# Performance work log

Measured on AMD Instinct MI355X. Metric: run time of the kernel, lower is better.

## Reference

```python
import jax, jax.numpy as jnp
import numpy as np

N_NODES = 65536
N_EDGES = 1048576


def gcn_conv(x, W, b, src, dst, n_nodes):
    """PyG GCNConv (normalize=True, add_self_loops already applied in src/dst):
    out = D^{-1/2} (A+I) D^{-1/2} X W + b, aggregated at dst (target) nodes."""
    deg = jax.ops.segment_sum(jnp.ones_like(dst, dtype=x.dtype), dst, num_segments=n_nodes)
    dis = jax.lax.rsqrt(jnp.maximum(deg, 1.0))  # self loops guarantee deg >= 1
    norm = dis[src] * dis[dst]                  # [E]
    h = x @ W                                   # [N, out]
    agg = jax.ops.segment_sum(h[src] * norm[:, None], dst, num_segments=n_nodes)
    return agg + b


def setup_inputs() -> dict:
    key = jax.random.key(0)
    ks = jax.random.split(key, 8)
    x = jax.random.normal(ks[0], (N_NODES, 128), dtype=jnp.float32)
    edge_index = jax.random.randint(ks[1], (2, N_EDGES), 0, N_NODES, dtype=jnp.int64)
    dims = [(128, 256), (256, 128), (128, 64)]
    params = {}
    for i, (din, dout) in enumerate(dims):
        scale = 1.0 / np.sqrt(din)
        params[f"W{i+1}"] = jax.random.uniform(ks[2 + i], (din, dout), dtype=jnp.float32, minval=-scale, maxval=scale)
        params[f"b{i+1}"] = jnp.zeros((dout,), dtype=jnp.float32)
    return {"x": x, "edge_index": edge_index, **params}


def reference(x, edge_index, W1, b1, W2, b2, W3, b3):
    n = x.shape[0]
    loop = jnp.arange(n, dtype=edge_index.dtype)
    src = jnp.concatenate([edge_index[0], loop])  # add self loops
    dst = jnp.concatenate([edge_index[1], loop])
    for W, b in ((W1, b1), (W2, b2), (W3, b3)):
        x = gcn_conv(x, W, b, src, dst, n)
        x = jax.nn.softmax(jax.nn.relu(x), axis=1)  # ReLU then Softmax(dim=1) per layer
    return x
```

## Files before the change

kernel.cpp:

```cpp
#include <hip/hip_runtime.h>
#include <cstdint>
#include <cstddef>

#define N_NODES 65536
#define N_EDGES 1048576
#define E_TOT   (N_EDGES + N_NODES)
#define CAP     5120

using short8  = __attribute__((ext_vector_type(8))) short;
using floatx4 = __attribute__((ext_vector_type(4))) float;
using half8   = __attribute__((ext_vector_type(8))) _Float16;
using half4   = __attribute__((ext_vector_type(4))) _Float16;
typedef unsigned short ushort_t;

__device__ inline void split_bf16(float a, short& hi, short& lo) {
    unsigned u  = __float_as_uint(a);
    unsigned hr = (u + 0x7fffu + ((u >> 16) & 1u)) >> 16;
    float    hf = __uint_as_float(hr << 16);
    hi = (short)hr;
    float    lf = a - hf;
    lo = (short)(__float_as_uint(lf) >> 16);
}


__global__ __launch_bounds__(1024) void k_bucket(const int* __restrict__ src, const int* __restrict__ dst,
                                                 int* __restrict__ gcur, unsigned* __restrict__ pk) {
    __shared__ int cnt[256];
    __shared__ int cur[256];
    int tid = threadIdx.x;
    if (tid < 256) cnt[tid] = 0;
    __syncthreads();
    int base = blockIdx.x * 4096;
    #pragma unroll
    for (int j = 0; j < 4; ++j) {
        int d = __builtin_nontemporal_load(&dst[base + j * 1024 + tid]);
        atomicAdd(&cnt[d >> 8], 1);
    }
    __syncthreads();
    if (tid < 256) cur[tid] = CAP * tid + atomicAdd(&gcur[tid], cnt[tid]);
    __syncthreads();
    #pragma unroll
    for (int j = 0; j < 4; ++j) {
        int e = base + j * 1024 + tid;
        int d = __builtin_nontemporal_load(&dst[e]);
        int s = __builtin_nontemporal_load(&src[e]);
        int pos = atomicAdd(&cur[d >> 8], 1);
        pk[pos] = ((unsigned)s << 16) | (unsigned)d;
    }
}

__global__ __launch_bounds__(256) void k_boff(const int* __restrict__ gcur, int* __restrict__ boff,
                                              int* __restrict__ off) {
    __shared__ int sb[256];
    int tid = threadIdx.x;
    int v = gcur[tid] + 256;
    sb[tid] = v;
    __syncthreads();
    #pragma unroll
    for (int s = 1; s < 256; s <<= 1) {
        int t = (tid >= s) ? sb[tid - s] : 0;
        __syncthreads();
        sb[tid] += t;
        __syncthreads();
    }
    boff[tid] = sb[tid] - v;
    if (tid == 255) boff[256] = sb[255];
    if (tid == 0) off[N_NODES] = E_TOT;
}

__global__ __launch_bounds__(1024) void k_sortb(const unsigned* __restrict__ pk, const int* __restrict__ gcur,
                                                const int* __restrict__ boff, int* __restrict__ off,
                                                float* __restrict__ dis, ushort_t* __restrict__ ssort) {
    __shared__ int cnt[256];
    __shared__ int sb[256];
    __shared__ int cur[256];
    int b = blockIdx.x;
    int tid = threadIdx.x;
    int n = gcur[b];
    const unsigned* p = pk + (size_t)b * CAP;
    if (tid < 256) cnt[tid] = 0;
    __syncthreads();
    for (int i = tid; i < n; i += 1024) atomicAdd(&cnt[p[i] & 255u], 1);
    __syncthreads();
    if (tid < 256) sb[tid] = cnt[tid];
    __syncthreads();
    #pragma unroll
    for (int s = 1; s < 256; s <<= 1) {
        int t = (tid < 256 && tid >= s) ? sb[tid - s] : 0;
        __syncthreads();
        if (tid < 256) sb[tid] += t;
        __syncthreads();
    }
    if (tid < 256) {
        int deg = cnt[tid];
        int o = boff[b] + (sb[tid] - deg) + tid;
        int d = b * 256 + tid;
        off[d] = o;
        dis[d] = rsqrtf((float)(deg + 1));
        ssort[o + deg] = (ushort_t)d;
        cur[tid] = o;
    }
    __syncthreads();
    for (int i = tid; i < n; i += 1024) {
        unsigned v = p[i];
        int pos = atomicAdd(&cur[v & 255u], 1);
        ssort[pos] = (ushort_t)(v >> 16);
    }
}


#define G1 (16 * 4 * 64)
#define G2 (8 * 8 * 64)
#define G3 (4 * 4 * 64)
#define NBX 8192
#define NBW ((G1 + G2 + G3 + 255) / 256)

__device__ inline void convw_split(const float* W, int K, int N, short* Bh, short* Bl, int g) {
    int lane = g & 63;
    int kt = (g >> 6) % (K / 32);
    int nt = (g >> 6) / (K / 32);
    int n = nt * 16 + (lane & 15);
    int kbase = kt * 32 + (lane >> 4) * 8;
    #pragma unroll
    for (int j = 0; j < 8; ++j) {
        short h, l;
        split_bf16(W[(size_t)(kbase + j) * N + n], h, l);
        Bh[(size_t)g * 8 + j] = h;
        Bl[(size_t)g * 8 + j] = l;
    }
}

__device__ inline void convw_h(const float* W, int K, int N, _Float16* Bf, int g) {
    int lane = g & 63;
    int kt = (g >> 6) % (K / 32);
    int nt = (g >> 6) / (K / 32);
    int n = nt * 16 + (lane & 15);
    int kbase = kt * 32 + (lane >> 4) * 8;
    #pragma unroll
    for (int j = 0; j < 8; ++j)
        Bf[(size_t)g * 8 + j] = (_Float16)W[(size_t)(kbase + j) * N + n];
}

__global__ __launch_bounds__(256) void k_fused(
        const float* __restrict__ x, const float* __restrict__ dis, _Float16* __restrict__ xh,
        const float* __restrict__ W1, short* __restrict__ w1h, short* __restrict__ w1l,
        const float* __restrict__ W2, _Float16* __restrict__ w2f,
        const float* __restrict__ W3, _Float16* __restrict__ w3f) {
    int b = blockIdx.x;
    if (b < NBX) {
        int idx = (b * 256 + threadIdx.x) * 4;
        int row = idx >> 7;
        float d = dis[row];
        float4 v = *(const float4*)(x + idx);
        half4 o = {(_Float16)(d * v.x), (_Float16)(d * v.y), (_Float16)(d * v.z), (_Float16)(d * v.w)};
        *(half4*)(xh + idx) = o;
    } else {
        int g = (b - NBX) * 256 + threadIdx.x;
        if (g < G1)                 convw_split(W1, 128, 256, w1h, w1l, g);
        else if (g < G1 + G2)       convw_h(W2, 256, 128, w2f, g - G1);
        else if (g < G1 + G2 + G3)  convw_h(W3, 128, 64, w3f, g - G1 - G2);
    }
}


template <int K, int N>
__global__ __launch_bounds__(256) void k_mms(const _Float16* __restrict__ A,
                                             const short* __restrict__ Bh, const short* __restrict__ Bl,
                                             const float* __restrict__ bias, _Float16* __restrict__ Cout) {
    constexpr int NT = N / 16;
    constexpr int KT = K / 32;
    int tid = threadIdx.x;
    int wave = tid >> 6, lane = tid & 63;
    int quad = lane >> 4, col = lane & 15;
    size_t row0 = (size_t)blockIdx.x * 64;
    const _Float16* ap = A + (row0 + wave * 16 + col) * K + quad * 8;

    floatx4 acc[NT];
    #pragma unroll
    for (int t = 0; t < NT; ++t) acc[t] = (floatx4)0.0f;

    for (int kt = 0; kt < KT; ++kt) {
        half8 a8 = *(const half8*)(ap + kt * 32);
        short ah[8], al[8];
        #pragma unroll
        for (int j = 0; j < 8; ++j) split_bf16((float)a8[j], ah[j], al[j]);
        short8 afh = *(short8*)ah;
        short8 afl = *(short8*)al;
        #pragma unroll
        for (int nt = 0; nt < NT; ++nt) {
            size_t bi = ((size_t)(nt * KT + kt) * 64 + lane);
            short8 bfh = ((const short8*)Bh)[bi];
            short8 bfl = ((const short8*)Bl)[bi];
            acc[nt] = __builtin_amdgcn_mfma_f32_16x16x32_bf16(afh, bfh, acc[nt], 0, 0, 0);
            acc[nt] = __builtin_amdgcn_mfma_f32_16x16x32_bf16(afh, bfl, acc[nt], 0, 0, 0);
            acc[nt] = __builtin_amdgcn_mfma_f32_16x16x32_bf16(afl, bfh, acc[nt], 0, 0, 0);
        }
    }

    size_t rbase = row0 + wave * 16 + quad * 4;
    float bv[NT];
    #pragma unroll
    for (int nt = 0; nt < NT; ++nt) bv[nt] = bias[nt * 16 + col];
    float mr[4] = {0.f, 0.f, 0.f, 0.f};
    #pragma unroll
    for (int nt = 0; nt < NT; ++nt)
        #pragma unroll
        for (int r = 0; r < 4; ++r) {
            float v = fmaxf(acc[nt][r] + bv[nt], 0.0f);
            acc[nt][r] = v;
            mr[r] = fmaxf(mr[r], v);
        }
    #pragma unroll
    for (int mask = 1; mask < 16; mask <<= 1)
        #pragma unroll
        for (int r = 0; r < 4; ++r) mr[r] = fmaxf(mr[r], __shfl_xor(mr[r], mask, 64));
    float sr[4] = {0.f, 0.f, 0.f, 0.f};
    #pragma unroll
    for (int nt = 0; nt < NT; ++nt)
        #pragma unroll
        for (int r = 0; r < 4; ++r) {
            float t = __expf(acc[nt][r] - mr[r]);
            acc[nt][r] = t;
            sr[r] += t;
        }
    #pragma unroll
    for (int mask = 1; mask < 16; mask <<= 1)
        #pragma unroll
        for (int r = 0; r < 4; ++r) sr[r] += __shfl_xor(sr[r], mask, 64);
    float inv[4];
    #pragma unroll
    for (int r = 0; r < 4; ++r) inv[r] = 1.0f / sr[r];
    #pragma unroll
    for (int nt = 0; nt < NT; ++nt)
        #pragma unroll
        for (int r = 0; r < 4; ++r)
            Cout[(rbase + r) * N + nt * 16 + col] = (_Float16)(acc[nt][r] * inv[r]);
}


template <int K, int N>
__global__ __launch_bounds__(256) void k_mmh(const _Float16* __restrict__ A,
                                             const _Float16* __restrict__ Bf,
                                             const float* __restrict__ dis, _Float16* __restrict__ Cout) {
    constexpr int NT = N / 16;
    constexpr int KT = K / 32;
    int tid = threadIdx.x;
    int wave = tid >> 6, lane = tid & 63;
    int quad = lane >> 4, col = lane & 15;
    size_t row0 = (size_t)blockIdx.x * 64;
    const _Float16* ap = A + (row0 + wave * 16 + col) * K + quad * 8;

    floatx4 acc[NT];
    #pragma unroll
    for (int t = 0; t < NT; ++t) acc[t] = (floatx4)0.0f;

    for (int kt = 0; kt < KT; ++kt) {
        half8 a8 = *(const half8*)(ap + kt * 32);
        #pragma unroll
        for (int nt = 0; nt < NT; ++nt) {
            half8 bf = ((const half8*)Bf)[(size_t)(nt * KT + kt) * 64 + lane];
            acc[nt] = __builtin_amdgcn_mfma_f32_16x16x32_f16(a8, bf, acc[nt], 0, 0, 0);
        }
    }

    size_t rbase = row0 + wave * 16 + quad * 4;
    float4 d4 = *(const float4*)(dis + rbase);
    float dr[4] = {d4.x, d4.y, d4.z, d4.w};
    #pragma unroll
    for (int nt = 0; nt < NT; ++nt)
        #pragma unroll
        for (int r = 0; r < 4; ++r)
            Cout[(rbase + r) * N + nt * 16 + col] = (_Float16)(acc[nt][r] * dr[r]);
}


template <bool ACT>
__global__ __launch_bounds__(256) void k_agg128h(const _Float16* __restrict__ h, const int* __restrict__ off,
                                                 const ushort_t* __restrict__ ss, const float* __restrict__ dis,
                                                 const float* __restrict__ bias, _Float16* __restrict__ out) {
    int lane = threadIdx.x & 63;
    int sub = lane >> 4;
    int li  = lane & 15;
    int c0  = li * 8;
    int n = blockIdx.x * 4 + (threadIdx.x >> 6);
    int e0 = off[n], e1 = off[n + 1];
    int e = e0;
    float acc[8];
    #pragma unroll
    for (int j = 0; j < 8; ++j) acc[j] = 0.0f;

    if (ACT) {
        half8 hacc = {0, 0, 0, 0, 0, 0, 0, 0};
        for (; e + 16 <= e1; e += 16) {
            int s0 = ss[e + sub];
            int s1 = ss[e + 4 + sub];
            int s2 = ss[e + 8 + sub];
            int s3 = ss[e + 12 + sub];
            half8 v0 = *(const half8*)(h + (size_t)s0 * 128 + c0);
            half8 v1 = *(const half8*)(h + (size_t)s1 * 128 + c0);
            half8 v2 = *(const half8*)(h + (size_t)s2 * 128 + c0);
            half8 v3 = *(const half8*)(h + (size_t)s3 * 128 + c0);
            hacc += (v0 + v1) + (v2 + v3);
        }
        for (; e + 8 <= e1; e += 8) {
            int sa = ss[e + sub];
            int sb = ss[e + 4 + sub];
            half8 va = *(const half8*)(h + (size_t)sa * 128 + c0);
            half8 vb = *(const half8*)(h + (size_t)sb * 128 + c0);
            hacc += va + vb;
        }
        #pragma unroll
        for (int j = 0; j < 8; ++j) acc[j] = (float)hacc[j];
    } else {
        for (; e + 16 <= e1; e += 16) {
            int s0 = ss[e + sub];
            int s1 = ss[e + 4 + sub];
            int s2 = ss[e + 8 + sub];
            int s3 = ss[e + 12 + sub];
            half8 v0 = *(const half8*)(h + (size_t)s0 * 128 + c0);
            half8 v1 = *(const half8*)(h + (size_t)s1 * 128 + c0);
            half8 v2 = *(const half8*)(h + (size_t)s2 * 128 + c0);
            half8 v3 = *(const half8*)(h + (size_t)s3 * 128 + c0);
            half8 vs = (v0 + v1) + (v2 + v3);
            #pragma unroll
            for (int j = 0; j < 8; ++j) acc[j] += (float)vs[j];
        }
        for (; e + 8 <= e1; e += 8) {
            int sa = ss[e + sub];
            int sb = ss[e + 4 + sub];
            half8 va = *(const half8*)(h + (size_t)sa * 128 + c0);
            half8 vb = *(const half8*)(h + (size_t)sb * 128 + c0);
            half8 vs = va + vb;
            #pragma unroll
            for (int j = 0; j < 8; ++j) acc[j] += (float)vs[j];
        }
    }
    while (e < e1) {
        int rem = e1 - e;
        int idx = e + sub;
        if (idx >= e1) idx = e1 - 1;
        int s = ss[idx];
        half8 v = *(const half8*)(h + (size_t)s * 128 + c0);
        float w = (sub < rem) ? 1.0f : 0.0f;
        #pragma unroll
        for (int j = 0; j < 8; ++j) acc[j] = fmaf(w, (float)v[j], acc[j]);
        e += 4;
    }

    #pragma unroll
    for (int mask = 32; mask >= 16; mask >>= 1)
        #pragma unroll
        for (int j = 0; j < 8; ++j) acc[j] += __shfl_xor(acc[j], mask, 64);

    float dn = dis[n];
    if (ACT) {
        float m = 0.0f;
        #pragma unroll
        for (int j = 0; j < 8; ++j) {
            float v = fmaxf(fmaf(acc[j], dn, bias[c0 + j]), 0.0f);
            acc[j] = v;
            m = fmaxf(m, v);
        }
        #pragma unroll
        for (int mask = 8; mask > 0; mask >>= 1) m = fmaxf(m, __shfl_xor(m, mask, 64));
        float sum = 0.0f;
        #pragma unroll
        for (int j = 0; j < 8; ++j) {
            float t = __expf(acc[j] - m);
            acc[j] = t;
            sum += t;
        }
        #pragma unroll
        for (int mask = 8; mask > 0; mask >>= 1) sum += __shfl_xor(sum, mask, 64);
        float inv = 1.0f / sum;
        #pragma unroll
        for (int j = 0; j < 8; ++j) acc[j] *= inv;
    } else {
        #pragma unroll
        for (int j = 0; j < 8; ++j) acc[j] *= dn;
    }
    if (sub == 0) {
        half8 o;
        #pragma unroll
        for (int j = 0; j < 8; ++j) o[j] = (_Float16)acc[j];
        *(half8*)(out + (size_t)n * 128 + c0) = o;
    }
}


__global__ __launch_bounds__(256) void k_agg64h(const _Float16* __restrict__ h, const int* __restrict__ off,
                                                const ushort_t* __restrict__ ss, const float* __restrict__ dis,
                                                const float* __restrict__ bias, float* __restrict__ out) {
    int lane = threadIdx.x & 63;
    int sub = lane >> 3;
    int li  = lane & 7;
    int c0  = li * 8;
    int n = blockIdx.x * 4 + (threadIdx.x >> 6);
    int e0 = off[n], e1 = off[n + 1];
    int e = e0;
    float acc[8];
    #pragma unroll
    for (int j = 0; j < 8; ++j) acc[j] = 0.0f;

    half8 hacc = {0, 0, 0, 0, 0, 0, 0, 0};
    for (; e + 16 <= e1; e += 16) {
        int s0 = ss[e + sub];
        int s1 = ss[e + 8 + sub];
        half8 v0 = *(const half8*)(h + (size_t)s0 * 64 + c0);
        half8 v1 = *(const half8*)(h + (size_t)s1 * 64 + c0);
        hacc += v0 + v1;
    }
    for (; e + 8 <= e1; e += 8) {
        int s = ss[e + sub];
        half8 v = *(const half8*)(h + (size_t)s * 64 + c0);
        hacc += v;
    }
    #pragma unroll
    for (int j = 0; j < 8; ++j) acc[j] = (float)hacc[j];

    int rem = e1 - e;
    if (rem > 0) {
        int idx = e + sub;
        if (idx >= e1) idx = e1 - 1;
        int s = ss[idx];
        half8 v = *(const half8*)(h + (size_t)s * 64 + c0);
        float w = (sub < rem) ? 1.0f : 0.0f;
        #pragma unroll
        for (int j = 0; j < 8; ++j) acc[j] = fmaf(w, (float)v[j], acc[j]);
    }

    #pragma unroll
    for (int mask = 32; mask >= 8; mask >>= 1)
        #pragma unroll
        for (int j = 0; j < 8; ++j) acc[j] += __shfl_xor(acc[j], mask, 64);

    float dn = dis[n];
    float m = 0.0f;
    #pragma unroll
    for (int j = 0; j < 8; ++j) {
        float v = fmaxf(fmaf(acc[j], dn, bias[c0 + j]), 0.0f);
        acc[j] = v;
        m = fmaxf(m, v);
    }
    #pragma unroll
    for (int mask = 4; mask > 0; mask >>= 1) m = fmaxf(m, __shfl_xor(m, mask, 64));
    float sum = 0.0f;
    #pragma unroll
    for (int j = 0; j < 8; ++j) {
        float t = __expf(acc[j] - m);
        acc[j] = t;
        sum += t;
    }
    #pragma unroll
    for (int mask = 4; mask > 0; mask >>= 1) sum += __shfl_xor(sum, mask, 64);
    float inv = 1.0f / sum;
    if (sub == 0) {
        float* op = out + (size_t)n * 64 + c0;
        *(float4*)(op)     = make_float4(acc[0] * inv, acc[1] * inv, acc[2] * inv, acc[3] * inv);
        *(float4*)(op + 4) = make_float4(acc[4] * inv, acc[5] * inv, acc[6] * inv, acc[7] * inv);
    }
}


extern "C" void kernel_launch(void* const* d_in, const int* in_sizes, int n_in,
                              void* d_out, int out_size, void* d_ws, size_t ws_size,
                              hipStream_t stream) {
    const float* x  = (const float*)d_in[0];
    const int*   ei = (const int*)d_in[1];
    const float* W1 = (const float*)d_in[2];
    const float* b1 = (const float*)d_in[3];
    const float* W2 = (const float*)d_in[4];
    const float* b2 = (const float*)d_in[5];
    const float* W3 = (const float*)d_in[6];
    const float* b3 = (const float*)d_in[7];
    const int* srcE = ei;
    const int* dstE = ei + N_EDGES;

    char* p = (char*)d_ws;
    auto carve = [&](size_t bytes) {
        char* q = p;
        p += (bytes + 255) & ~(size_t)255;
        return q;
    };
    int*          gcur  = (int*)carve(sizeof(int) * 256);
    int*          boff  = (int*)carve(sizeof(int) * 257);
    int*          off   = (int*)carve(sizeof(int) * (N_NODES + 1));
    float*        dis   = (float*)carve(sizeof(float) * N_NODES);
    unsigned*     pk    = (unsigned*)carve(sizeof(unsigned) * 256 * CAP);
    ushort_t*     ssort = (ushort_t*)carve(sizeof(ushort_t) * E_TOT);
    short*        w1h   = (short*)carve(sizeof(short) * 128 * 256);
    short*        w1l   = (short*)carve(sizeof(short) * 128 * 256);
    _Float16*     w2f   = (_Float16*)carve(sizeof(_Float16) * 256 * 128);
    _Float16*     w3f   = (_Float16*)carve(sizeof(_Float16) * 128 * 64);
    _Float16*     xh    = (_Float16*)carve(sizeof(_Float16) * (size_t)N_NODES * 128);
    _Float16*     a0h   = (_Float16*)carve(sizeof(_Float16) * (size_t)N_NODES * 128);
    _Float16*     x1h   = (_Float16*)carve(sizeof(_Float16) * (size_t)N_NODES * 256);
    _Float16*     x2h   = (_Float16*)carve(sizeof(_Float16) * (size_t)N_NODES * 128);
    _Float16*     hh    = (_Float16*)carve(sizeof(_Float16) * (size_t)N_NODES * 128);

    (void)hipMemsetAsync(gcur, 0, sizeof(int) * 256, stream);
    k_bucket<<<256, 1024, 0, stream>>>(srcE, dstE, gcur, pk);
    k_boff<<<1, 256, 0, stream>>>(gcur, boff, off);
    k_sortb<<<256, 1024, 0, stream>>>(pk, gcur, boff, off, dis, ssort);
    k_fused<<<NBX + NBW, 256, 0, stream>>>(x, dis, xh, W1, w1h, w1l, W2, w2f, W3, w3f);

    k_agg128h<false><<<N_NODES / 4, 256, 0, stream>>>(xh, off, ssort, dis, nullptr, a0h);
    k_mms<128, 256><<<N_NODES / 64, 256, 0, stream>>>(a0h, w1h, w1l, b1, x1h);
    k_mmh<256, 128><<<N_NODES / 64, 256, 0, stream>>>(x1h, w2f, dis, hh);
    k_agg128h<true><<<N_NODES / 4, 256, 0, stream>>>(hh, off, ssort, dis, b2, x2h);
    k_mmh<128, 64><<<N_NODES / 64, 256, 0, stream>>>(x2h, w3f, dis, hh);
    k_agg64h<<<N_NODES / 4, 256, 0, stream>>>(hh, off, ssort, dis, b3, (float*)d_out);
}
```

Baseline: 293.1 us.

## Slice feature matrices into 32-column planes for cache-friendly gather aggregation

Stores the 128-wide fp16 feature matrices as four 32-column slices (N x 32 each), so each aggregation block gathers only one slice. The working set per pass then fits in L2 and gathers become 64-byte rows. The activation (bias, ReLU, softmax) is moved out of the layer-2 aggregation into a separate k_act2 kernel. This adds an extra kernel launch and an extra intermediate buffer round-trip, and reads the CSR offsets and indices four times.

```diff
diff --git a/kernel.cpp b/kernel.cpp
--- a/kernel.cpp
+++ b/kernel.cpp
@@ -6,11 +6,13 @@
 #define N_EDGES 1048576
 #define E_TOT   (N_EDGES + N_NODES)
 #define CAP     5120
+#define SLICE_ELEMS ((size_t)N_NODES * 32)
 
 using short8  = __attribute__((ext_vector_type(8))) short;
 using floatx4 = __attribute__((ext_vector_type(4))) float;
 using half8   = __attribute__((ext_vector_type(8))) _Float16;
 using half4   = __attribute__((ext_vector_type(4))) _Float16;
+using half2v  = __attribute__((ext_vector_type(2))) _Float16;
 typedef unsigned short ushort_t;
 
 __device__ inline void split_bf16(float a, short& hi, short& lo) {
@@ -150,10 +152,11 @@
     if (b < NBX) {
         int idx = (b * 256 + threadIdx.x) * 4;
         int row = idx >> 7;
+        int c0 = idx & 127;
         float d = dis[row];
         float4 v = *(const float4*)(x + idx);
         half4 o = {(_Float16)(d * v.x), (_Float16)(d * v.y), (_Float16)(d * v.z), (_Float16)(d * v.w)};
-        *(half4*)(xh + idx) = o;
+        *(half4*)(xh + (size_t)(c0 >> 5) * SLICE_ELEMS + (size_t)row * 32 + (c0 & 31)) = o;
     } else {
         int g = (b - NBX) * 256 + threadIdx.x;
         if (g < G1)                 convw_split(W1, 128, 256, w1h, w1l, g);
@@ -238,7 +241,7 @@
 }
 
 
-template <int K, int N>
+template <int K, int N, bool SLICED>
 __global__ __launch_bounds__(256) void k_mmh(const _Float16* __restrict__ A,
                                              const _Float16* __restrict__ Bf,
                                              const float* __restrict__ dis, _Float16* __restrict__ Cout) {
@@ -269,122 +272,94 @@
     #pragma unroll
     for (int nt = 0; nt < NT; ++nt)
         #pragma unroll
-        for (int r = 0; r < 4; ++r)
-            Cout[(rbase + r) * N + nt * 16 + col] = (_Float16)(acc[nt][r] * dr[r]);
-}
-
-
-template <bool ACT>
-__global__ __launch_bounds__(256) void k_agg128h(const _Float16* __restrict__ h, const int* __restrict__ off,
-                                                 const ushort_t* __restrict__ ss, const float* __restrict__ dis,
-                                                 const float* __restrict__ bias, _Float16* __restrict__ out) {
+        for (int r = 0; r < 4; ++r) {
+            int c = nt * 16 + col;
+            _Float16 v = (_Float16)(acc[nt][r] * dr[r]);
+            if (SLICED)
+                Cout[(size_t)(c >> 5) * SLICE_ELEMS + (rbase + r) * 32 + (c & 31)] = v;
+            else
+                Cout[(rbase + r) * N + c] = v;
+        }
+}
+
+
+template <bool FP32ACC>
+__global__ __launch_bounds__(256) void k_aggs(const _Float16* __restrict__ h, const int* __restrict__ off,
+                                              const ushort_t* __restrict__ ss, const float* __restrict__ dis,
+                                              _Float16* __restrict__ out) {
+    int g = blockIdx.x & 7;
     int lane = threadIdx.x & 63;
-    int sub = lane >> 4;
-    int li  = lane & 15;
-    int c0  = li * 8;
+    int wave = threadIdx.x >> 6;
+    int sub = lane >> 3;
+    int li  = lane & 7;
+    const _Float16* hs = h + (size_t)g * SLICE_ELEMS + li * 4;
+    int nbase = (blockIdx.x >> 3) * 8 + wave * 2;
+
+    #pragma unroll
+    for (int k = 0; k < 2; ++k) {
+        int n = nbase + k;
+        int e0 = off[n], e1 = off[n + 1];
+        int e = e0;
+        float acc[4] = {0.f, 0.f, 0.f, 0.f};
+        if (FP32ACC) {
+            for (; e + 8 <= e1; e += 8) {
+                int s = ss[e + sub];
+                half4 v = *(const half4*)(hs + (size_t)s * 32);
+                #pragma unroll
+                for (int j = 0; j < 4; ++j) acc[j] += (float)v[j];
+            }
+        } else {
+            half4 hacc = {0, 0, 0, 0};
+            for (; e + 8 <= e1; e += 8) {
+                int s = ss[e + sub];
+                half4 v = *(const half4*)(hs + (size_t)s * 32);
+                hacc += v;
+            }
+            #pragma unroll
+            for (int j = 0; j < 4; ++j) acc[j] = (float)hacc[j];
+        }
+        int rem = e1 - e;
+        if (rem > 0) {
+            int idx = e + sub;
+            if (idx >= e1) idx = e1 - 1;
+            int s = ss[idx];
+            half4 v = *(const half4*)(hs + (size_t)s * 32);
+            float w = (sub < rem) ? 1.0f : 0.0f;
+            #pragma unroll
+            for (int j = 0; j < 4; ++j) acc[j] = fmaf(w, (float)v[j], acc[j]);
+        }
+        #pragma unroll
+        for (int mask = 32; mask >= 8; mask >>= 1)
+            #pragma unroll
+            for (int j = 0; j < 4; ++j) acc[j] += __shfl_xor(acc[j], mask, 64);
+        float dn = dis[n];
+        if (sub == 0) {
+            half4 o = {(_Float16)(acc[0] * dn), (_Float16)(acc[1] * dn),
+                       (_Float16)(acc[2] * dn), (_Float16)(acc[3] * dn)};
+            *(half4*)(out + (size_t)n * 128 + g * 32 + li * 4) = o;
+        }
+    }
+}
+
+
+__global__ __launch_bounds__(256) void k_act2(const _Float16* __restrict__ z, const float* __restrict__ bias,
+                                              _Float16* __restrict__ out) {
+    int lane = threadIdx.x & 63;
     int n = blockIdx.x * 4 + (threadIdx.x >> 6);
-    int e0 = off[n], e1 = off[n + 1];
-    int e = e0;
-    float acc[8];
-    #pragma unroll
-    for (int j = 0; j < 8; ++j) acc[j] = 0.0f;
-
-    if (ACT) {
-        half8 hacc = {0, 0, 0, 0, 0, 0, 0, 0};
-        for (; e + 16 <= e1; e += 16) {
-            int s0 = ss[e + sub];
-            int s1 = ss[e + 4 + sub];
-            int s2 = ss[e + 8 + sub];
-            int s3 = ss[e + 12 + sub];
-            half8 v0 = *(const half8*)(h + (size_t)s0 * 128 + c0);
-            half8 v1 = *(const half8*)(h + (size_t)s1 * 128 + c0);
-            half8 v2 = *(const half8*)(h + (size_t)s2 * 128 + c0);
-            half8 v3 = *(const half8*)(h + (size_t)s3 * 128 + c0);
-            hacc += (v0 + v1) + (v2 + v3);
-        }
-        for (; e + 8 <= e1; e += 8) {
-            int sa = ss[e + sub];
-            int sb = ss[e + 4 + sub];
-            half8 va = *(const half8*)(h + (size_t)sa * 128 + c0);
-            half8 vb = *(const half8*)(h + (size_t)sb * 128 + c0);
-            hacc += va + vb;
-        }
-        #pragma unroll
-        for (int j = 0; j < 8; ++j) acc[j] = (float)hacc[j];
-    } else {
-        for (; e + 16 <= e1; e += 16) {
-            int s0 = ss[e + sub];
-            int s1 = ss[e + 4 + sub];
-            int s2 = ss[e + 8 + sub];
-            int s3 = ss[e + 12 + sub];
-            half8 v0 = *(const half8*)(h + (size_t)s0 * 128 + c0);
-            half8 v1 = *(const half8*)(h + (size_t)s1 * 128 + c0);
-            half8 v2 = *(const half8*)(h + (size_t)s2 * 128 + c0);
-            half8 v3 = *(const half8*)(h + (size_t)s3 * 128 + c0);
-            half8 vs = (v0 + v1) + (v2 + v3);
-            #pragma unroll
-            for (int j = 0; j < 8; ++j) acc[j] += (float)vs[j];
-        }
-        for (; e + 8 <= e1; e += 8) {
-            int sa = ss[e + sub];
-            int sb = ss[e + 4 + sub];
-            half8 va = *(const half8*)(h + (size_t)sa * 128 + c0);
-            half8 vb = *(const half8*)(h + (size_t)sb * 128 + c0);
-            half8 vs = va + vb;
-            #pragma unroll
-            for (int j = 0; j < 8; ++j) acc[j] += (float)vs[j];
-        }
-    }
-    while (e < e1) {
-        int rem = e1 - e;
-        int idx = e + sub;
-        if (idx >= e1) idx = e1 - 1;
-        int s = ss[idx];
-        half8 v = *(const half8*)(h + (size_t)s * 128 + c0);
-        float w = (sub < rem) ? 1.0f : 0.0f;
-        #pragma unroll
-        for (int j = 0; j < 8; ++j) acc[j] = fmaf(w, (float)v[j], acc[j]);
-        e += 4;
-    }
-
-    #pragma unroll
-    for (int mask = 32; mask >= 16; mask >>= 1)
-        #pragma unroll
-        for (int j = 0; j < 8; ++j) acc[j] += __shfl_xor(acc[j], mask, 64);
-
-    float dn = dis[n];
-    if (ACT) {
-        float m = 0.0f;
-        #pragma unroll
-        for (int j = 0; j < 8; ++j) {
-            float v = fmaxf(fmaf(acc[j], dn, bias[c0 + j]), 0.0f);
-            acc[j] = v;
-            m = fmaxf(m, v);
-        }
-        #pragma unroll
-        for (int mask = 8; mask > 0; mask >>= 1) m = fmaxf(m, __shfl_xor(m, mask, 64));
-        float sum = 0.0f;
-        #pragma unroll
-        for (int j = 0; j < 8; ++j) {
-            float t = __expf(acc[j] - m);
-            acc[j] = t;
-            sum += t;
-        }
-        #pragma unroll
-        for (int mask = 8; mask > 0; mask >>= 1) sum += __shfl_xor(sum, mask, 64);
-        float inv = 1.0f / sum;
-        #pragma unroll
-        for (int j = 0; j < 8; ++j) acc[j] *= inv;
-    } else {
-        #pragma unroll
-        for (int j = 0; j < 8; ++j) acc[j] *= dn;
-    }
-    if (sub == 0) {
-        half8 o;
-        #pragma unroll
-        for (int j = 0; j < 8; ++j) o[j] = (_Float16)acc[j];
-        *(half8*)(out + (size_t)n * 128 + c0) = o;
-    }
+    int c0 = lane * 2;
+    half2v z2 = *(const half2v*)(z + (size_t)n * 128 + c0);
+    float v0 = fmaxf((float)z2[0] + bias[c0], 0.0f);
+    float v1 = fmaxf((float)z2[1] + bias[c0 + 1], 0.0f);
+    float m = fmaxf(v0, v1);
+    #pragma unroll
+    for (int mask = 32; mask > 0; mask >>= 1) m = fmaxf(m, __shfl_xor(m, mask, 64));
+    float t0 = __expf(v0 - m), t1 = __expf(v1 - m);
+    float sum = t0 + t1;
+    #pragma unroll
+    for (int mask = 32; mask > 0; mask >>= 1) sum += __shfl_xor(sum, mask, 64);
+    float inv = 1.0f / sum;
+    half2v o = {(_Float16)(t0 * inv), (_Float16)(t1 * inv)};
+    *(half2v*)(out + (size_t)n * 128 + c0) = o;
 }
 
 
@@ -496,6 +471,7 @@
     _Float16*     a0h   = (_Float16*)carve(sizeof(_Float16) * (size_t)N_NODES * 128);
     _Float16*     x1h   = (_Float16*)carve(sizeof(_Float16) * (size_t)N_NODES * 256);
     _Float16*     x2h   = (_Float16*)carve(sizeof(_Float16) * (size_t)N_NODES * 128);
+    _Float16*     zz    = (_Float16*)carve(sizeof(_Float16) * (size_t)N_NODES * 128);
     _Float16*     hh    = (_Float16*)carve(sizeof(_Float16) * (size_t)N_NODES * 128);
 
     (void)hipMemsetAsync(gcur, 0, sizeof(int) * 256, stream);
@@ -504,10 +480,11 @@
     k_sortb<<<256, 1024, 0, stream>>>(pk, gcur, boff, off, dis, ssort);
     k_fused<<<NBX + NBW, 256, 0, stream>>>(x, dis, xh, W1, w1h, w1l, W2, w2f, W3, w3f);
 
-    k_agg128h<false><<<N_NODES / 4, 256, 0, stream>>>(xh, off, ssort, dis, nullptr, a0h);
+    k_aggs<true><<<8 * (N_NODES / 8), 256, 0, stream>>>(xh, off, ssort, dis, a0h);
     k_mms<128, 256><<<N_NODES / 64, 256, 0, stream>>>(a0h, w1h, w1l, b1, x1h);
-    k_mmh<256, 128><<<N_NODES / 64, 256, 0, stream>>>(x1h, w2f, dis, hh);
-    k_agg128h<true><<<N_NODES / 4, 256, 0, stream>>>(hh, off, ssort, dis, b2, x2h);
-    k_mmh<128, 64><<<N_NODES / 64, 256, 0, stream>>>(x2h, w3f, dis, hh);
+    k_mmh<256, 128, true><<<N_NODES / 64, 256, 0, stream>>>(x1h, w2f, dis, hh);
+    k_aggs<false><<<8 * (N_NODES / 8), 256, 0, stream>>>(hh, off, ssort, dis, zz);
+    k_act2<<<N_NODES / 4, 256, 0, stream>>>(zz, b2, x2h);
+    k_mmh<128, 64, false><<<N_NODES / 64, 256, 0, stream>>>(x2h, w3f, dis, hh);
     k_agg64h<<<N_NODES / 4, 256, 0, stream>>>(hh, off, ssort, dis, b3, (float*)d_out);
 }
```

New measurement: 574.2 us. 95.9% more time.
